# Performance work log

Hardware: AMD Instinct MI355X
Metric: run time of the kernel (lower is better)

The kernel has to match this reference:

```python
import jax, jax.numpy as jnp
import numpy as np

# Social pooling hyperparameters (from init_kwargs config)
INFLUENCE_RADIUS = 10.0
SIGMA = 5.0
MAX_NEIGHBORS = 32
COORD_SCALE = 100.0  # coordinates uniform in [0, 100)^2


def setup_inputs() -> dict:
    key = jax.random.key(0)
    k1, k2 = jax.random.split(key)
    B, N, D = 8, 8192, 64
    features = jax.random.normal(k1, (B, N, D), dtype=jnp.float32)
    coordinates = jax.random.uniform(k2, (N, 2), dtype=jnp.float32) * COORD_SCALE
    return {"features": features, "coordinates": coordinates}


def _spatial_weights(coordinates):
    # Pairwise squared Euclidean distances [N, N]
    diff = coordinates[:, None, :] - coordinates[None, :, :]
    d2 = jnp.sum(diff * diff, axis=-1)
    d = jnp.sqrt(jnp.maximum(d2, 1e-12))
    # Gaussian kernel with hard radius cutoff
    w = jnp.exp(-d2 / (2.0 * SIGMA * SIGMA))
    w = jnp.where(d <= INFLUENCE_RADIUS, w, 0.0)
    # Neighbor limit: keep top-k weights per row
    topk_vals, _ = jax.lax.top_k(w, MAX_NEIGHBORS)  # [N, K]
    thresh = topk_vals[:, -1:]
    w = jnp.where(w >= thresh, w, 0.0)
    # weighted_mean normalization
    row_sums = jnp.clip(jnp.sum(w, axis=1, keepdims=True), 1e-8, None)
    return w / row_sums


def reference(features, coordinates):
    # features: [B, N, D]; coordinates: [N, 2]
    weights = _spatial_weights(coordinates)          # [N, N]
    pooled = jnp.einsum('ij,bjd->bid', weights, features)
    return pooled  # aggregation_layer is Identity (learnable_aggregation=False)
```

## Files before the change

### kernel.cpp

```cpp
#include <hip/hip_runtime.h>
#include <math.h>


constexpr int   NCELL  = 10;
constexpr int   NCELL2 = 100;
constexpr int   MAXC   = 416;
constexpr int   MAXK   = 64;
constexpr float BUCKSC = 2.56f;
constexpr int   NXCD   = 8;

__device__ __forceinline__ int cell_x(float x) {
    int c = (int)(x * 0.09765625f);
    return min(max(c, 0), NCELL - 1);
}
__device__ __forceinline__ int cell_of(float2 c) {
    return cell_x(c.y) * NCELL + cell_x(c.x);
}

__device__ __forceinline__ void wsync() {
    __builtin_amdgcn_wave_barrier();
    asm volatile("s_waitcnt lgkmcnt(0)" ::: "memory");
    __builtin_amdgcn_wave_barrier();
}

__global__ __launch_bounds__(1024)
void k_prep(const float* __restrict__ C, int* __restrict__ cellStart,
            float2* __restrict__ bXY, int* __restrict__ bIdx, int N)
{
    __shared__ int h[128];
    __shared__ int cur[NCELL2];
    const int t = threadIdx.x;
    if (t < 128) h[t] = 0;
    __syncthreads();
    const float2* C2 = (const float2*)C;
    for (int j = t; j < N; j += 1024) atomicAdd(&h[cell_of(C2[j])], 1);
    __syncthreads();
    #pragma unroll
    for (int o = 1; o < 128; o <<= 1) {
        int u = (t < 128 && t >= o) ? h[t - o] : 0;
        __syncthreads();
        if (t < 128) h[t] += u;
        __syncthreads();
    }
    if (t < NCELL2) {
        int s = (t == 0) ? 0 : h[t - 1];
        cur[t] = s; cellStart[t] = s;
        if (t == 0) cellStart[NCELL2] = h[NCELL2 - 1];
    }
    __syncthreads();
    for (int j = t; j < N; j += 1024) {
        float2 c = C2[j];
        int pos = atomicAdd(&cur[cell_of(c)], 1);
        bXY[pos] = c; bIdx[pos] = j;
    }
}

template<int TN, int TB>
__global__ __launch_bounds__(256, 8)
void social_pool_main(const float* __restrict__ F,
                      const float2* __restrict__ bXY,
                      const int* __restrict__ bIdx,
                      const int* __restrict__ cellStart,
                      float* __restrict__ out, int Nrt, int Brt)
{
    const int N = (TN > 0) ? TN : Nrt;
    const int B = (TB > 0) ? TB : Brt;

    __shared__ float  s_cd2[4][MAXC];
    __shared__ int    s_cjj[4][MAXC];
    __shared__ __align__(16) int s_hist[4][256];
    __shared__ float  s_blist[4][32];
    __shared__ float2 s_kwj[4][MAXK];

    const int t = threadIdx.x, wid = t >> 6, lane = t & 63;
    float*  cd2   = s_cd2[wid];
    int*    cjj   = s_cjj[wid];
    int*    hist  = s_hist[wid];
    float*  blist = s_blist[wid];
    float2* kwj   = s_kwj[wid];

    *(int4*)&hist[lane * 4] = make_int4(0, 0, 0, 0);

    const int bid = blockIdx.x, nb = gridDim.x;
    int q;
    if (TN > 0) {
        q = (bid & 7) * 1024 + wid * 256 + (bid >> 3);
    } else {
        const int sb = (nb % NXCD == 0) ? (bid % NXCD) * (nb / NXCD) + bid / NXCD : bid;
        q = sb * 4 + wid;
    }
    if (q >= N) return;

    const float2 ci = bXY[q];
    const int    i  = bIdx[q];
    const int cx = cell_x(ci.x), cy = cell_x(ci.y);
    const unsigned long long below = (1ull << lane) - 1ull;

    int mc = 0;
    for (int ry = max(cy - 1, 0); ry <= min(cy + 1, NCELL - 1); ++ry) {
        const int c0 = ry * NCELL + max(cx - 1, 0);
        const int c1 = ry * NCELL + min(cx + 1, NCELL - 1);
        const int s = cellStart[c0], e = cellStart[c1 + 1];
        for (int p0 = s; p0 < e; p0 += 64) {
            const int p = p0 + lane;
            bool hit = false; float d2 = 0.0f;
            if (p < e) {
                float2 cp = bXY[p];
                float dx = ci.x - cp.x, dy = ci.y - cp.y;
                d2 = dx * dx + dy * dy;
                float d = sqrtf(fmaxf(d2, 1e-12f));
                hit = (d <= 10.0f);
            }
            unsigned long long mk = __ballot(hit);
            int off = __popcll(mk & below);
            if (hit && mc + off < MAXC) { cd2[mc + off] = d2; cjj[mc + off] = p; }
            mc += (int)__popcll(mk);
        }
    }
    wsync();
    const int M = min(mc, MAXC);

    float thr_d2, thr_w;
    if (M > 32) {
        for (int k = lane; k < M; k += 64)
            atomicAdd(&hist[min(255, (int)(cd2[k] * BUCKSC))], 1);
        wsync();
        int4 h4 = *(const int4*)&hist[lane * 4];
        int hh0 = h4.x, hh1 = h4.y, hh2 = h4.z, hh3 = h4.w;
        int tot = hh0 + hh1 + hh2 + hh3;
        int sc = tot;
        #pragma unroll
        for (int o = 1; o < 64; o <<= 1) {
            int v = __shfl_up(sc, o);
            if (lane >= o) sc += v;
        }
        int ce = sc - tot;
        int fb = -1, fce = 0;
        if (ce <= 31 && 31 < ce + hh0) { fb = lane * 4 + 0; fce = ce; } ce += hh0;
        if (fb < 0 && ce <= 31 && 31 < ce + hh1) { fb = lane * 4 + 1; fce = ce; } ce += hh1;
        if (fb < 0 && ce <= 31 && 31 < ce + hh2) { fb = lane * 4 + 2; fce = ce; } ce += hh2;
        if (fb < 0 && ce <= 31 && 31 < ce + hh3) { fb = lane * 4 + 3; fce = ce; }
        unsigned long long mk1 = __ballot(fb >= 0);
        int src1 = (mk1 != 0ull) ? (__ffsll((unsigned long long)mk1) - 1) : 0;
        const int bstar   = __shfl(fb,  src1);
        const int cumexcl = __shfl(fce, src1);
        int bn = 0;
        for (int k0 = 0; k0 < M; k0 += 64) {
            const int k = k0 + lane;
            bool inb = (k < M) && (min(255, (int)(cd2[k] * BUCKSC)) == bstar);
            unsigned long long mk = __ballot(inb);
            int off = __popcll(mk & below);
            if (inb && bn + off < 32) blist[bn + off] = cd2[k];
            bn += (int)__popcll(mk);
        }
        wsync();
        bn = min(bn, 32);
        float mine = 0.0f; int ok = 0;
        if (lane < bn) {
            mine = blist[lane];
            int cl = 0, ceq = 0;
            for (int m = 0; m < bn; ++m) {
                cl  += (blist[m] <  mine);
                ceq += (blist[m] == mine);
            }
            int r = cumexcl + cl;
            ok = (r <= 31 && 31 < r + ceq);
        }
        unsigned long long mk2 = __ballot(ok);
        int src2 = (mk2 != 0ull) ? (__ffsll((unsigned long long)mk2) - 1) : 0;
        thr_d2 = __shfl(mine, src2);
        thr_w  = expf(-(thr_d2 / 50.0f));
    } else {
        thr_d2 = 3.4e38f;
        thr_w  = 0.0f;
    }

    const float marg = thr_d2 + 1e-4f;
    int kc = 0;
    for (int k0 = 0; k0 < M; k0 += 64) {
        const int k = k0 + lane;
        bool keep = false; float w = 0.0f; int jj = 0;
        if (k < M && cd2[k] <= marg) {
            w = expf(-(cd2[k] / 50.0f));
            if (w >= thr_w) { keep = true; jj = bIdx[cjj[k]]; }
        }
        unsigned long long mk = __ballot(keep);
        int off = __popcll(mk & below);
        if (keep && kc + off < MAXK)
            kwj[kc + off] = make_float2(w, __int_as_float(jj));
        kc += (int)__popcll(mk);
    }
    wsync();
    const int K = min(kc, MAXK);

    float2 pr = make_float2(0.0f, 0.0f);
    if (lane < K) pr = kwj[lane];
    float v = pr.x;
    #pragma unroll
    for (int o = 32; o > 0; o >>= 1) v += __shfl_xor(v, o);
    const float ssum = fmaxf(v, 1e-8f);
    const float wn = pr.x / ssum;
    const int   jn = __float_as_int(pr.y);
    const int   wi = __float_as_int(wn);

    const size_t NL = (size_t)N * 64;
    if (TB == 8) {
        const int dq = (lane & 15) * 4;
        const int bp = (lane >> 4) * 2;
        const float* Fb0 = F + (size_t)bp * NL + dq;
        const float* Fb1 = Fb0 + NL;
        float4 a0 = make_float4(0.f, 0.f, 0.f, 0.f);
        float4 a1 = make_float4(0.f, 0.f, 0.f, 0.f);
        #pragma unroll 2
        for (int k = 0; k < K; ++k) {
            const float w = __int_as_float(__builtin_amdgcn_readlane(wi, k));
            const size_t o = (size_t)__builtin_amdgcn_readlane(jn, k) * 64;
            float4 f0 = *(const float4*)(Fb0 + o);
            float4 f1 = *(const float4*)(Fb1 + o);
            a0.x += w * f0.x; a0.y += w * f0.y; a0.z += w * f0.z; a0.w += w * f0.w;
            a1.x += w * f1.x; a1.y += w * f1.y; a1.z += w * f1.z; a1.w += w * f1.w;
        }
        float* O0 = out + (size_t)bp * NL + (size_t)i * 64 + dq;
        *(float4*)O0 = a0;
        *(float4*)(O0 + NL) = a1;
    } else {
        const float* F0 = F + lane;
        float* O0 = out + (size_t)i * 64 + lane;
        for (int b = 0; b < B; ++b) {
            float a = 0.0f;
            const float* Fb = F0 + (size_t)b * NL;
            for (int k = 0; k < K; ++k) {
                const float w = __int_as_float(__builtin_amdgcn_readlane(wi, k));
                const size_t o = (size_t)__builtin_amdgcn_readlane(jn, k) * 64;
                a += w * Fb[o];
            }
            O0[(size_t)b * NL] = a;
        }
    }
}

extern "C" void kernel_launch(void* const* d_in, const int* in_sizes, int n_in,
                              void* d_out, int out_size, void* d_ws, size_t ws_size,
                              hipStream_t stream)
{
    const float* F = (const float*)d_in[0];
    const float* C = (const float*)d_in[1];
    float* out = (float*)d_out;

    const int N = in_sizes[1] / 2;
    const int B = in_sizes[0] / (N * 64);

    char* ws = (char*)d_ws;
    int*    cellStart = (int*)(ws + 0);
    float2* bXY       = (float2*)(ws + 512);
    int*    bIdx      = (int*)(ws + 512 + (size_t)N * 8);

    k_prep<<<1, 1024, 0, stream>>>(C, cellStart, bXY, bIdx, N);
    if (N == 8192 && B == 8)
        social_pool_main<8192, 8><<<2048, 256, 0, stream>>>(F, bXY, bIdx, cellStart, out, N, B);
    else
        social_pool_main<0, 0><<<(N + 3) / 4, 256, 0, stream>>>(F, bXY, bIdx, cellStart, out, N, B);
}
```

Before: 50.71 us.

## Permute features into cell-sorted order before gather for spatial locality

Adds a kernel that copies the feature tensor into cell-bucketed point order in workspace. The main kernel then gathers neighbor rows from this permuted buffer, so neighbors of nearby queries sit in contiguous memory and cache reuse improves. The fast path also switches the block-to-query mapping to the generic XCD-aware sb scheme. The cost is an extra 16MB read plus 16MB write pass and a dependency on workspace size.

```diff
diff --git a/kernel.cpp b/kernel.cpp
--- a/kernel.cpp
+++ b/kernel.cpp
@@ -55,9 +55,23 @@
     }
 }
 
-template<int TN, int TB>
+__global__ __launch_bounds__(256)
+void k_permute(const float* __restrict__ F, const int* __restrict__ bIdx,
+               float* __restrict__ FB)
+{
+    const int tid = blockIdx.x * 256 + threadIdx.x;
+    const int dq4 = tid & 15;
+    const int p   = (tid >> 4) & 8191;
+    const int b   = tid >> 17;
+    const int j   = bIdx[p];
+    const float4* src = (const float4*)(F  + ((size_t)b * 8192 + j) * 64) + dq4;
+    float4*       dst = (float4*)      (FB + ((size_t)b * 8192 + p) * 64) + dq4;
+    *dst = *src;
+}
+
+template<int TN, int TB, bool TFB>
 __global__ __launch_bounds__(256, 8)
-void social_pool_main(const float* __restrict__ F,
+void social_pool_main(const float* __restrict__ FG,
                       const float2* __restrict__ bXY,
                       const int* __restrict__ bIdx,
                       const int* __restrict__ cellStart,
@@ -82,13 +96,8 @@
     *(int4*)&hist[lane * 4] = make_int4(0, 0, 0, 0);
 
     const int bid = blockIdx.x, nb = gridDim.x;
-    int q;
-    if (TN > 0) {
-        q = (bid & 7) * 1024 + wid * 256 + (bid >> 3);
-    } else {
-        const int sb = (nb % NXCD == 0) ? (bid % NXCD) * (nb / NXCD) + bid / NXCD : bid;
-        q = sb * 4 + wid;
-    }
+    const int sb = (nb % NXCD == 0) ? (bid % NXCD) * (nb / NXCD) + bid / NXCD : bid;
+    const int q = sb * 4 + wid;
     if (q >= N) return;
 
     const float2 ci = bXY[q];
@@ -182,7 +191,7 @@
         bool keep = false; float w = 0.0f; int jj = 0;
         if (k < M && cd2[k] <= marg) {
             w = expf(-(cd2[k] / 50.0f));
-            if (w >= thr_w) { keep = true; jj = bIdx[cjj[k]]; }
+            if (w >= thr_w) { keep = true; jj = TFB ? cjj[k] : bIdx[cjj[k]]; }
         }
         unsigned long long mk = __ballot(keep);
         int off = __popcll(mk & below);
@@ -207,7 +216,7 @@
     if (TB == 8) {
         const int dq = (lane & 15) * 4;
         const int bp = (lane >> 4) * 2;
-        const float* Fb0 = F + (size_t)bp * NL + dq;
+        const float* Fb0 = FG + (size_t)bp * NL + dq;
         const float* Fb1 = Fb0 + NL;
         float4 a0 = make_float4(0.f, 0.f, 0.f, 0.f);
         float4 a1 = make_float4(0.f, 0.f, 0.f, 0.f);
@@ -224,7 +233,7 @@
         *(float4*)O0 = a0;
         *(float4*)(O0 + NL) = a1;
     } else {
-        const float* F0 = F + lane;
+        const float* F0 = FG + lane;
         float* O0 = out + (size_t)i * 64 + lane;
         for (int b = 0; b < B; ++b) {
             float a = 0.0f;
@@ -254,10 +263,19 @@
     int*    cellStart = (int*)(ws + 0);
     float2* bXY       = (float2*)(ws + 512);
     int*    bIdx      = (int*)(ws + 512 + (size_t)N * 8);
+    size_t  base      = 512 + (size_t)N * 8 + (size_t)N * 4;
+    size_t  fbOff     = (base + 255) & ~(size_t)255;
+    float*  FB        = (float*)(ws + fbOff);
+    const size_t needFast = fbOff + (size_t)N * B * 64 * sizeof(float);
 
     k_prep<<<1, 1024, 0, stream>>>(C, cellStart, bXY, bIdx, N);
-    if (N == 8192 && B == 8)
-        social_pool_main<8192, 8><<<2048, 256, 0, stream>>>(F, bXY, bIdx, cellStart, out, N, B);
-    else
-        social_pool_main<0, 0><<<(N + 3) / 4, 256, 0, stream>>>(F, bXY, bIdx, cellStart, out, N, B);
-}
+
+    if (N == 8192 && B == 8 && ws_size >= needFast) {
+        k_permute<<<4096, 256, 0, stream>>>(F, bIdx, FB);
+        social_pool_main<8192, 8, true><<<2048, 256, 0, stream>>>(
+            FB, bXY, bIdx, cellStart, out, N, B);
+    } else {
+        social_pool_main<0, 0, false><<<(N + 3) / 4, 256, 0, stream>>>(
+            F, bXY, bIdx, cellStart, out, N, B);
+    }
+}
```

Measured after the change: 61.92 us. 1.22x slower.

## Split pooling into permute, neighbor-select and gather kernels with cell-sorted feature layout

Applied to the files above, without the earlier changes.

Replaces the single fused kernel with three kernels. The first permutes features into cell-sorted, batch-interleaved rows so each neighbor's 8x64 block is contiguous. The second computes top-k neighbor weights per point and writes them to workspace. The third gathers from the permuted layout with better spatial locality. The aim is to improve gather locality and coalescing, at the cost of an extra full feature copy (16 MB read plus write), two extra launches and workspace traffic for the neighbor lists.

```diff
diff --git a/kernel.cpp b/kernel.cpp
--- a/kernel.cpp
+++ b/kernel.cpp
@@ -55,17 +55,28 @@
     }
 }
 
-template<int TN, int TB>
+__global__ __launch_bounds__(256)
+void k_permute(const float* __restrict__ F, const int* __restrict__ bIdx,
+               float* __restrict__ FB2)
+{
+    const int t  = blockIdx.x * 256 + threadIdx.x;
+    const int p  = t >> 7;
+    const int r  = t & 127;
+    const int b  = r >> 4;
+    const int dq = r & 15;
+    const int j  = bIdx[p];
+    const float4 v = ((const float4*)(F + ((size_t)b * 8192 + (size_t)j) * 64))[dq];
+    ((float4*)(FB2 + (size_t)p * 512 + b * 64))[dq] = v;
+}
+
 __global__ __launch_bounds__(256, 8)
-void social_pool_main(const float* __restrict__ F,
-                      const float2* __restrict__ bXY,
-                      const int* __restrict__ bIdx,
-                      const int* __restrict__ cellStart,
-                      float* __restrict__ out, int Nrt, int Brt)
-{
-    const int N = (TN > 0) ? TN : Nrt;
-    const int B = (TB > 0) ? TB : Brt;
-
+void k_select(const float2* __restrict__ bXY,
+              const int* __restrict__ bIdx,
+              const int* __restrict__ cellStart,
+              float2* __restrict__ kv,
+              int2* __restrict__ kn,
+              int N)
+{
     __shared__ float  s_cd2[4][MAXC];
     __shared__ int    s_cjj[4][MAXC];
     __shared__ __align__(16) int s_hist[4][256];
@@ -82,13 +93,8 @@
     *(int4*)&hist[lane * 4] = make_int4(0, 0, 0, 0);
 
     const int bid = blockIdx.x, nb = gridDim.x;
-    int q;
-    if (TN > 0) {
-        q = (bid & 7) * 1024 + wid * 256 + (bid >> 3);
-    } else {
-        const int sb = (nb % NXCD == 0) ? (bid % NXCD) * (nb / NXCD) + bid / NXCD : bid;
-        q = sb * 4 + wid;
-    }
+    const int sb = (nb % NXCD == 0) ? (bid % NXCD) * (nb / NXCD) + bid / NXCD : bid;
+    const int q = sb * 4 + wid;
     if (q >= N) return;
 
     const float2 ci = bXY[q];
@@ -182,6 +188,189 @@
         bool keep = false; float w = 0.0f; int jj = 0;
         if (k < M && cd2[k] <= marg) {
             w = expf(-(cd2[k] / 50.0f));
+            if (w >= thr_w) { keep = true; jj = cjj[k]; }
+        }
+        unsigned long long mk = __ballot(keep);
+        int off = __popcll(mk & below);
+        if (keep && kc + off < MAXK)
+            kwj[kc + off] = make_float2(w, __int_as_float(jj));
+        kc += (int)__popcll(mk);
+    }
+    wsync();
+    const int K = min(kc, MAXK);
+
+    float2 pr = make_float2(0.0f, 0.0f);
+    if (lane < K) pr = kwj[lane];
+    float v = pr.x;
+    #pragma unroll
+    for (int o = 32; o > 0; o >>= 1) v += __shfl_xor(v, o);
+    const float ssum = fmaxf(v, 1e-8f);
+    const float wn = pr.x / ssum;
+
+    kv[(size_t)q * MAXK + lane] =
+        (lane < K) ? make_float2(wn, pr.y) : make_float2(0.0f, __int_as_float(0));
+    if (lane == 0) kn[q] = make_int2((K + 3) & ~3, i);
+}
+
+__global__ __launch_bounds__(256)
+void k_pool(const float* __restrict__ FB2,
+            const float2* __restrict__ kv,
+            const int2* __restrict__ kn,
+            float* __restrict__ out)
+{
+    const int wid = threadIdx.x >> 6, lane = threadIdx.x & 63;
+    const int c = blockIdx.x & 7;
+    const int l = blockIdx.x >> 3;
+    const int b  = lane >> 3;
+    const int d8 = (lane & 7) * 8;
+    const size_t NL = (size_t)8192 * 64;
+
+    for (int ph = 0; ph < 4; ++ph) {
+        const int row = c * 1024 + ph * 256 + l * 4 + wid;
+        const int2 kni = kn[row];
+        const int Kp = kni.x;
+        const int i  = kni.y;
+        const float2 prl = kv[(size_t)row * MAXK + lane];
+        const int wi = __float_as_int(prl.x);
+        const int pi = __float_as_int(prl.y);
+        float4 a0 = make_float4(0.f, 0.f, 0.f, 0.f);
+        float4 a1 = make_float4(0.f, 0.f, 0.f, 0.f);
+        for (int k = 0; k < Kp; k += 4) {
+            #pragma unroll
+            for (int u = 0; u < 4; ++u) {
+                const float w = __int_as_float(__builtin_amdgcn_readlane(wi, k + u));
+                const int   p = __builtin_amdgcn_readlane(pi, k + u);
+                const float* s = FB2 + (size_t)p * 512 + b * 64 + d8;
+                float4 f0 = *(const float4*)s;
+                float4 f1 = *(const float4*)(s + 4);
+                a0.x += w * f0.x; a0.y += w * f0.y; a0.z += w * f0.z; a0.w += w * f0.w;
+                a1.x += w * f1.x; a1.y += w * f1.y; a1.z += w * f1.z; a1.w += w * f1.w;
+            }
+        }
+        float* O = out + (size_t)b * NL + (size_t)i * 64 + d8;
+        *(float4*)O = a0;
+        *(float4*)(O + 4) = a1;
+    }
+}
+
+__global__ __launch_bounds__(256, 8)
+void social_pool_fused(const float* __restrict__ F,
+                       const float2* __restrict__ bXY,
+                       const int* __restrict__ bIdx,
+                       const int* __restrict__ cellStart,
+                       float* __restrict__ out, int N, int B)
+{
+    __shared__ float  s_cd2[4][MAXC];
+    __shared__ int    s_cjj[4][MAXC];
+    __shared__ __align__(16) int s_hist[4][256];
+    __shared__ float  s_blist[4][32];
+    __shared__ float2 s_kwj[4][MAXK];
+
+    const int t = threadIdx.x, wid = t >> 6, lane = t & 63;
+    float*  cd2   = s_cd2[wid];
+    int*    cjj   = s_cjj[wid];
+    int*    hist  = s_hist[wid];
+    float*  blist = s_blist[wid];
+    float2* kwj   = s_kwj[wid];
+
+    *(int4*)&hist[lane * 4] = make_int4(0, 0, 0, 0);
+
+    const int bid = blockIdx.x, nb = gridDim.x;
+    const int sb = (nb % NXCD == 0) ? (bid % NXCD) * (nb / NXCD) + bid / NXCD : bid;
+    const int q = sb * 4 + wid;
+    if (q >= N) return;
+
+    const float2 ci = bXY[q];
+    const int    i  = bIdx[q];
+    const int cx = cell_x(ci.x), cy = cell_x(ci.y);
+    const unsigned long long below = (1ull << lane) - 1ull;
+
+    int mc = 0;
+    for (int ry = max(cy - 1, 0); ry <= min(cy + 1, NCELL - 1); ++ry) {
+        const int c0 = ry * NCELL + max(cx - 1, 0);
+        const int c1 = ry * NCELL + min(cx + 1, NCELL - 1);
+        const int s = cellStart[c0], e = cellStart[c1 + 1];
+        for (int p0 = s; p0 < e; p0 += 64) {
+            const int p = p0 + lane;
+            bool hit = false; float d2 = 0.0f;
+            if (p < e) {
+                float2 cp = bXY[p];
+                float dx = ci.x - cp.x, dy = ci.y - cp.y;
+                d2 = dx * dx + dy * dy;
+                float d = sqrtf(fmaxf(d2, 1e-12f));
+                hit = (d <= 10.0f);
+            }
+            unsigned long long mk = __ballot(hit);
+            int off = __popcll(mk & below);
+            if (hit && mc + off < MAXC) { cd2[mc + off] = d2; cjj[mc + off] = p; }
+            mc += (int)__popcll(mk);
+        }
+    }
+    wsync();
+    const int M = min(mc, MAXC);
+
+    float thr_d2, thr_w;
+    if (M > 32) {
+        for (int k = lane; k < M; k += 64)
+            atomicAdd(&hist[min(255, (int)(cd2[k] * BUCKSC))], 1);
+        wsync();
+        int4 h4 = *(const int4*)&hist[lane * 4];
+        int hh0 = h4.x, hh1 = h4.y, hh2 = h4.z, hh3 = h4.w;
+        int tot = hh0 + hh1 + hh2 + hh3;
+        int sc = tot;
+        #pragma unroll
+        for (int o = 1; o < 64; o <<= 1) {
+            int v = __shfl_up(sc, o);
+            if (lane >= o) sc += v;
+        }
+        int ce = sc - tot;
+        int fb = -1, fce = 0;
+        if (ce <= 31 && 31 < ce + hh0) { fb = lane * 4 + 0; fce = ce; } ce += hh0;
+        if (fb < 0 && ce <= 31 && 31 < ce + hh1) { fb = lane * 4 + 1; fce = ce; } ce += hh1;
+        if (fb < 0 && ce <= 31 && 31 < ce + hh2) { fb = lane * 4 + 2; fce = ce; } ce += hh2;
+        if (fb < 0 && ce <= 31 && 31 < ce + hh3) { fb = lane * 4 + 3; fce = ce; }
+        unsigned long long mk1 = __ballot(fb >= 0);
+        int src1 = (mk1 != 0ull) ? (__ffsll((unsigned long long)mk1) - 1) : 0;
+        const int bstar   = __shfl(fb,  src1);
+        const int cumexcl = __shfl(fce, src1);
+        int bn = 0;
+        for (int k0 = 0; k0 < M; k0 += 64) {
+            const int k = k0 + lane;
+            bool inb = (k < M) && (min(255, (int)(cd2[k] * BUCKSC)) == bstar);
+            unsigned long long mk = __ballot(inb);
+            int off = __popcll(mk & below);
+            if (inb && bn + off < 32) blist[bn + off] = cd2[k];
+            bn += (int)__popcll(mk);
+        }
+        wsync();
+        bn = min(bn, 32);
+        float mine = 0.0f; int ok = 0;
+        if (lane < bn) {
+            mine = blist[lane];
+            int cl = 0, ceq = 0;
+            for (int m = 0; m < bn; ++m) {
+                cl  += (blist[m] <  mine);
+                ceq += (blist[m] == mine);
+            }
+            int r = cumexcl + cl;
+            ok = (r <= 31 && 31 < r + ceq);
+        }
+        unsigned long long mk2 = __ballot(ok);
+        int src2 = (mk2 != 0ull) ? (__ffsll((unsigned long long)mk2) - 1) : 0;
+        thr_d2 = __shfl(mine, src2);
+        thr_w  = expf(-(thr_d2 / 50.0f));
+    } else {
+        thr_d2 = 3.4e38f;
+        thr_w  = 0.0f;
+    }
+
+    const float marg = thr_d2 + 1e-4f;
+    int kc = 0;
+    for (int k0 = 0; k0 < M; k0 += 64) {
+        const int k = k0 + lane;
+        bool keep = false; float w = 0.0f; int jj = 0;
+        if (k < M && cd2[k] <= marg) {
+            w = expf(-(cd2[k] / 50.0f));
             if (w >= thr_w) { keep = true; jj = bIdx[cjj[k]]; }
         }
         unsigned long long mk = __ballot(keep);
@@ -204,38 +393,17 @@
     const int   wi = __float_as_int(wn);
 
     const size_t NL = (size_t)N * 64;
-    if (TB == 8) {
-        const int dq = (lane & 15) * 4;
-        const int bp = (lane >> 4) * 2;
-        const float* Fb0 = F + (size_t)bp * NL + dq;
-        const float* Fb1 = Fb0 + NL;
-        float4 a0 = make_float4(0.f, 0.f, 0.f, 0.f);
-        float4 a1 = make_float4(0.f, 0.f, 0.f, 0.f);
-        #pragma unroll 2
+    const float* F0 = F + lane;
+    float* O0 = out + (size_t)i * 64 + lane;
+    for (int b = 0; b < B; ++b) {
+        float a = 0.0f;
+        const float* Fb = F0 + (size_t)b * NL;
         for (int k = 0; k < K; ++k) {
             const float w = __int_as_float(__builtin_amdgcn_readlane(wi, k));
             const size_t o = (size_t)__builtin_amdgcn_readlane(jn, k) * 64;
-            float4 f0 = *(const float4*)(Fb0 + o);
-            float4 f1 = *(const float4*)(Fb1 + o);
-            a0.x += w * f0.x; a0.y += w * f0.y; a0.z += w * f0.z; a0.w += w * f0.w;
-            a1.x += w * f1.x; a1.y += w * f1.y; a1.z += w * f1.z; a1.w += w * f1.w;
-        }
-        float* O0 = out + (size_t)bp * NL + (size_t)i * 64 + dq;
-        *(float4*)O0 = a0;
-        *(float4*)(O0 + NL) = a1;
-    } else {
-        const float* F0 = F + lane;
-        float* O0 = out + (size_t)i * 64 + lane;
-        for (int b = 0; b < B; ++b) {
-            float a = 0.0f;
-            const float* Fb = F0 + (size_t)b * NL;
-            for (int k = 0; k < K; ++k) {
-                const float w = __int_as_float(__builtin_amdgcn_readlane(wi, k));
-                const size_t o = (size_t)__builtin_amdgcn_readlane(jn, k) * 64;
-                a += w * Fb[o];
-            }
-            O0[(size_t)b * NL] = a;
-        }
+            a += w * Fb[o];
+        }
+        O0[(size_t)b * NL] = a;
     }
 }
 
@@ -254,10 +422,22 @@
     int*    cellStart = (int*)(ws + 0);
     float2* bXY       = (float2*)(ws + 512);
     int*    bIdx      = (int*)(ws + 512 + (size_t)N * 8);
+    size_t  off       = 512 + (size_t)N * 8 + (size_t)N * 4;
+    off = (off + 15) & ~(size_t)15;
+    int2*   kn        = (int2*)(ws + off);   off += (size_t)N * 8;
+    float2* kv        = (float2*)(ws + off); off += (size_t)N * MAXK * 8;
+    off = (off + 255) & ~(size_t)255;
+    float*  FB2       = (float*)(ws + off);
+    const size_t needFast = off + (size_t)N * B * 64 * sizeof(float);
 
     k_prep<<<1, 1024, 0, stream>>>(C, cellStart, bXY, bIdx, N);
-    if (N == 8192 && B == 8)
-        social_pool_main<8192, 8><<<2048, 256, 0, stream>>>(F, bXY, bIdx, cellStart, out, N, B);
-    else
-        social_pool_main<0, 0><<<(N + 3) / 4, 256, 0, stream>>>(F, bXY, bIdx, cellStart, out, N, B);
-}
+
+    if (N == 8192 && B == 8 && ws_size >= needFast) {
+        k_permute<<<4096, 256, 0, stream>>>(F, bIdx, FB2);
+        k_select <<<2048, 256, 0, stream>>>(bXY, bIdx, cellStart, kv, kn, N);
+        k_pool   <<< 512, 256, 0, stream>>>(FB2, kv, kn, out);
+    } else {
+        social_pool_fused<<<(N + 3) / 4, 256, 0, stream>>>(
+            F, bXY, bIdx, cellStart, out, N, B);
+    }
+}
```

After: 69.66 us. 1.37x slower.
